# Optimization experiments

Measured on AMD Instinct MI355X. Metric: run time of the kernel, lower is better.

The kernel has to match this reference:

```python
import jax, jax.numpy as jnp
import numpy as np

# Dims: T=out_seq_len, B=batch, D=hidden_dim, H=hidden_dim_de, E=embedding_size, C=feat_channels
T, B, D, H, E, C, FH, FW = 32, 16, 512, 512, 512, 512, 8, 32


def _lstm_dir(x_seq, W_ih, W_hh, b_ih, b_hh, reverse):
    # x_seq: (T, B, D); PyTorch gate order i, f, g, o
    gx = jnp.einsum('tbd,gd->tbg', x_seq, W_ih) + b_ih  # (T, B, 4H)
    Hh = W_hh.shape[1]
    def step(carry, g_t):
        h, c = carry
        g = g_t + h @ W_hh.T + b_hh
        i, f, gg, o = jnp.split(g, 4, axis=-1)
        c = jax.nn.sigmoid(f) * c + jax.nn.sigmoid(i) * jnp.tanh(gg)
        h = jax.nn.sigmoid(o) * jnp.tanh(c)
        return (h, c), h
    init = (jnp.zeros((x_seq.shape[1], Hh), x_seq.dtype),
            jnp.zeros((x_seq.shape[1], Hh), x_seq.dtype))
    _, hs = jax.lax.scan(step, init, gx, reverse=reverse)
    return hs  # (T, B, H)


def setup_inputs() -> dict:
    key = jax.random.key(0)
    ks = jax.random.split(key, 16)
    s = 0.02
    inp = {
        'hidden_en': jax.random.normal(ks[0], (T, B, D), jnp.float32),
        'conv_f': jax.random.normal(ks[1], (B, C, FH, FW), jnp.float32),
        # bidirectional LSTM params (PyTorch layout: W_ih (4H, D), W_hh (4H, H))
        'W_ih_f': jax.random.normal(ks[2], (4 * H, D), jnp.float32) * s,
        'W_hh_f': jax.random.normal(ks[3], (4 * H, H), jnp.float32) * s,
        'b_ih_f': jnp.zeros((4 * H,), jnp.float32),
        'b_hh_f': jnp.zeros((4 * H,), jnp.float32),
        'W_ih_b': jax.random.normal(ks[4], (4 * H, D), jnp.float32) * s,
        'W_hh_b': jax.random.normal(ks[5], (4 * H, H), jnp.float32) * s,
        'b_ih_b': jnp.zeros((4 * H,), jnp.float32),
        'b_hh_b': jnp.zeros((4 * H,), jnp.float32),
        # linear_decode: (H, 2H)
        'W_dec': jax.random.normal(ks[6], (H, 2 * H), jnp.float32) * s,
        'b_dec': jnp.zeros((H,), jnp.float32),
        # conv_em: 3x3, C -> E (OIHW)
        'W_em': jax.random.normal(ks[7], (E, C, 3, 3), jnp.float32) * s,
        'b_em': jnp.zeros((E,), jnp.float32),
        # attention h_em: 1x1 conv == linear H -> E
        'W_hem': jax.random.normal(ks[8], (E, H), jnp.float32) * s,
        'b_hem': jnp.zeros((E,), jnp.float32),
        # conv_att: 1x1 conv E -> 1
        'w_att': jax.random.normal(ks[9], (E,), jnp.float32) * s,
        'b_att': jnp.zeros((), jnp.float32),
    }
    return inp


def reference(hidden_en, conv_f, W_ih_f, W_hh_f, b_ih_f, b_hh_f,
              W_ih_b, W_hh_b, b_ih_b, b_hh_b, W_dec, b_dec,
              W_em, b_em, W_hem, b_hem, w_att, b_att):
    # decoder_ctc: bidirectional LSTM + linear
    h_fwd = _lstm_dir(hidden_en, W_ih_f, W_hh_f, b_ih_f, b_hh_f, reverse=False)
    h_bwd = _lstm_dir(hidden_en, W_ih_b, W_hh_b, b_ih_b, b_hh_b, reverse=True)
    hidden_de = jnp.concatenate([h_fwd, h_bwd], axis=-1) @ W_dec.T + b_dec  # (T, B, H)

    # conv_em: 3x3 same-padding conv, NCHW
    x_em = jax.lax.conv_general_dilated(
        conv_f, W_em, window_strides=(1, 1), padding='SAME',
        dimension_numbers=('NCHW', 'OIHW', 'NCHW')) + b_em[None, :, None, None]  # (B,E,FH,FW)
    att_x_em = jnp.transpose(x_em.reshape(x_em.shape[0], E, -1), (0, 2, 1))  # (B, HW, E)

    # batched attention over all timesteps (dropout is identity at eval)
    h_em = jnp.einsum('tbh,eh->tbe', hidden_de, W_hem) + b_hem  # (T, B, E)
    feat = jnp.tanh(x_em[None] + h_em[:, :, :, None, None])     # (T, B, E, FH, FW)
    scores = jnp.einsum('tbehw,e->tbhw', feat, w_att) + b_att   # (T, B, FH, FW)
    alpha = jax.nn.softmax(scores.reshape(scores.shape[0], scores.shape[1], -1), axis=-1)  # (T,B,HW)
    att = jnp.einsum('tbn,bne->tbe', alpha, att_x_em)           # (T, B, E)

    ctc_out = jnp.concatenate([hidden_de, att], axis=-1)        # (T, B, H+E)
    return jnp.transpose(ctc_out, (1, 0, 2))                    # (B, T, H+E)
```

## Files before the change

### kernel.cpp

```cpp
#include <hip/hip_runtime.h>
#include <hip/hip_bf16.h>
#include <math.h>

#define T_LEN 32
#define BATCH 16
#define DDIM  512
#define HDIM  512
#define EDIM  512
#define CDIM  512
#define FHH   8
#define FWW   32
#define HW    256
#define G4    2048
#define PADH  10
#define PADW  34
#define WLP   520

typedef __attribute__((ext_vector_type(8))) short bf16x8;
typedef __attribute__((ext_vector_type(4))) float f32x4;
typedef __attribute__((ext_vector_type(4))) int i32x4;

__device__ __forceinline__ ushort bfr(float x) {
    union { float f; uint32_t u; } c; c.f = x;
    uint32_t r = (c.u + 0x7FFFu + ((c.u >> 16) & 1u)) >> 16;
    return (ushort)r;
}

__device__ __forceinline__ float frcp(float x) { return __builtin_amdgcn_rcpf(x); }
__device__ __forceinline__ float ftanh(float x) {
    return 1.f - 2.f * frcp(1.f + __expf(2.f * x));
}
__device__ __forceinline__ float fsig(float x) {
    return frcp(1.f + __expf(-x));
}

__device__ __forceinline__ void ld_lds16(const void* g, void* l) {
    __builtin_amdgcn_global_load_lds((const __attribute__((address_space(1))) void*)g,
                                     (__attribute__((address_space(3))) void*)l, 16, 0, 0);
}

__device__ __forceinline__ void st_u16_sc1(ushort* p, ushort v) {
    asm volatile("global_store_short %0, %1, off sc1" :: "v"(p), "v"((uint)v) : "memory");
}
__device__ __forceinline__ void st_i32_sc1(int* p, int v) {
    asm volatile("global_store_dword %0, %1, off sc1" :: "v"(p), "v"(v) : "memory");
}
__device__ __forceinline__ void st_f32_sc1(float* p, float v) {
    asm volatile("global_store_dword %0, %1, off sc1" :: "v"(p), "v"(v) : "memory");
}
__device__ __forceinline__ int ld_i32_sc1(const int* p) {
    int v;
    asm volatile("global_load_dword %0, %1, off sc1\n\ts_waitcnt vmcnt(0)"
                 : "=v"(v) : "v"(p) : "memory");
    return v;
}
__device__ __forceinline__ i32x4 ld_i32x4_sc1(const int* p) {
    i32x4 v;
    asm volatile("global_load_dwordx4 %0, %1, off sc1\n\ts_waitcnt vmcnt(0)"
                 : "=v"(v) : "v"(p) : "memory");
    return v;
}
__device__ __forceinline__ float ld_f32_sc1(const float* p) {
    float v;
    asm volatile("global_load_dword %0, %1, off sc1\n\ts_waitcnt vmcnt(0)"
                 : "=v"(v) : "v"(p) : "memory");
    return v;
}
__device__ __forceinline__ f32x4 ld_f32x4_sc1_async(const float* p) {
    f32x4 v;
    asm volatile("global_load_dwordx4 %0, %1, off sc1" : "=v"(v) : "v"(p));
    return v;
}

struct PrepArgs { const float* s[7]; ushort* d[7]; };
__global__ __launch_bounds__(256) void prep_all(
    PrepArgs a, int* __restrict__ syncbuf,
    const float* __restrict__ conv_f, ushort* __restrict__ padT,
    const float* __restrict__ W_em, ushort* __restrict__ Wt,
    const float* __restrict__ W_dec, ushort* __restrict__ WdecT,
    const float* __restrict__ W_hem, const float* __restrict__ b_dec,
    const float* __restrict__ b_hem, float* __restrict__ b_comb)
{
    __shared__ float tile[32][33];
    const int bid = blockIdx.x, tid = threadIdx.x;
    if (bid < 5120) {
        int i = bid * 256 + tid;
        if (i < 128) st_i32_sc1(syncbuf + i, 0);
        const int e0 = 65536, e1 = 327680, e2 = 589824, e3 = 851968,
                  e4 = 1114112, e5 = 1245184;
        int seg, base;
        if      (i < e0) { seg = 0; base = 0;  }
        else if (i < e1) { seg = 1; base = e0; }
        else if (i < e2) { seg = 2; base = e1; }
        else if (i < e3) { seg = 3; base = e2; }
        else if (i < e4) { seg = 4; base = e3; }
        else if (i < e5) { seg = 5; base = e4; }
        else             { seg = 6; base = e5; }
        int li = i - base;
        float4 v = ((const float4*)a.s[seg])[li];
        ushort4 o;
        o.x = bfr(v.x); o.y = bfr(v.y); o.z = bfr(v.z); o.w = bfr(v.w);
        ((ushort4*)a.d[seg])[li] = o;
        return;
    }
    if (bid < 7168) {
        int id = bid - 5120;
        int s0 = (id & 7) * 32, c0 = ((id >> 3) & 15) * 32, b = id >> 7;
        int lo = tid & 31, hi = tid >> 5;
#pragma unroll
        for (int it = 0; it < 4; ++it) {
            int cl = hi + it * 8;
            tile[cl][lo] = conv_f[((size_t)(b * CDIM + c0 + cl)) * HW + s0 + lo];
        }
        __syncthreads();
#pragma unroll
        for (int it = 0; it < 4; ++it) {
            int sl = hi + it * 8;
            int s = s0 + sl;
            int y = s >> 5, x = s & 31;
            padT[(((size_t)b * PADH + y + 1) * PADW + (x + 1)) * CDIM + c0 + lo] =
                bfr(tile[lo][sl]);
        }
        return;
    }
    if (bid < 7840) {
        int gid = (bid - 7168) * 256 + tid;
        int c4 = gid & 127;
        int cellb = gid >> 7;
        int cell = cellb % 84;
        int b = cellb / 84;
        int y, x;
        if (cell < 34) { y = 0; x = cell; }
        else if (cell < 68) { y = 9; x = cell - 34; }
        else { int k2 = cell - 68; y = 1 + (k2 >> 1); x = (k2 & 1) ? 33 : 0; }
        ((ushort4*)padT)[(((size_t)b * PADH + y) * PADW + x) * (CDIM / 4) + c4] =
            make_ushort4(0, 0, 0, 0);
        return;
    }
    if (bid < 17056) {
        int gid = (bid - 7840) * 256 + tid;
        int c = gid % CDIM;
        int t = gid / CDIM;
        int e = t % EDIM;
        int tap = t / EDIM;
        int dy = tap / 3, dx = tap % 3;
        Wt[gid] = bfr(W_em[((e * CDIM + c) * 3 + dy) * 3 + dx]);
        return;
    }
    if (bid < 17568) {
        int idx = bid - 17056;
        int ht = idx & 15, kt = idx >> 4;
        int h0 = ht * 32, k0 = kt * 32;
        int lo = tid & 31, hi = tid >> 5;
#pragma unroll
        for (int it = 0; it < 4; ++it) {
            int i = hi + it * 8;
            tile[i][lo] = W_dec[(size_t)(h0 + i) * 1024 + k0 + lo];
        }
        __syncthreads();
#pragma unroll
        for (int it = 0; it < 4; ++it) {
            int i = hi + it * 8;
            WdecT[(size_t)(k0 + i) * 512 + h0 + lo] = bfr(tile[lo][i]);
        }
        return;
    }
    {
        int e = (bid - 17568) * 256 + tid;
        float s = b_hem[e];
        const float* wr = W_hem + (size_t)e * 512;
        for (int h = 0; h < 512; ++h) s += wr[h] * b_dec[h];
        b_comb[e] = s;
    }
}

__device__ __forceinline__ void tile64_compute(
    const ushort* Ap0, const ushort* Bp0, int K,
    ushort* smem, int tid, f32x4 (&acc)[2][2])
{
    ushort* As = smem;
    ushort* Bs = smem + 2048;
    const int w = tid >> 6, lane = tid & 63;
    ushort* AsW = &As[w * 512];
    ushort* BsW = &Bs[w * 512];
    const int wm = (w >> 1) * 32, wn = (w & 1) * 32;
    const int kb = (lane >> 4) * 8, fr = lane & 15;
    for (int kk = 0; kk < K; kk += 32) {
        __syncthreads();
        ld_lds16(Ap0 + kk, AsW);
        ld_lds16(Bp0 + kk, BsW);
        __syncthreads();
        bf16x8 af[2], bg[2];
#pragma unroll
        for (int i = 0; i < 2; ++i)
            af[i] = *(const bf16x8*)&As[(wm + i * 16 + fr) * 32 + kb];
#pragma unroll
        for (int j = 0; j < 2; ++j)
            bg[j] = *(const bf16x8*)&Bs[(wn + j * 16 + fr) * 32 + kb];
#pragma unroll
        for (int i = 0; i < 2; ++i)
#pragma unroll
            for (int j = 0; j < 2; ++j)
                acc[i][j] = __builtin_amdgcn_mfma_f32_16x16x32_bf16(af[i], bg[j], acc[i][j], 0, 0, 0);
    }
}

__global__ __launch_bounds__(256) void fused_main(
    const ushort* __restrict__ Whh_f, const ushort* __restrict__ Whh_b,
    float* __restrict__ gxT_f, float* __restrict__ gxT_b,
    const ushort* __restrict__ hen_bf,
    const ushort* __restrict__ Wih_f, const ushort* __restrict__ Wih_b,
    const float* __restrict__ b_ih_f, const float* __restrict__ b_hh_f,
    const float* __restrict__ b_ih_b, const float* __restrict__ b_hh_b,
    ushort* __restrict__ hs_bf,
    int* __restrict__ syncbuf,
    const ushort* __restrict__ padT, const ushort* __restrict__ Wt,
    const float* __restrict__ bias_em, float* __restrict__ xem,
    const ushort* __restrict__ Whem_bf, const ushort* __restrict__ WdecT_bf,
    ushort* __restrict__ Wcomb_bf)
{
    __shared__ ushort smem[49152];
    const int bid = blockIdx.x, tid = threadIdx.x;
    const int w = tid >> 6, lane = tid & 63;
    int* flags = syncbuf;
    int* gcnt  = syncbuf + 64;

    if (bid < 64) {
        const int dir = bid >> 5;
        const int j0 = (bid & 31) * 16;
        const ushort* W = dir ? Whh_b : Whh_f;
        const float* gx = dir ? gxT_b : gxT_f;
#pragma unroll
        for (int i = 0; i < 16; ++i) {
            int row = w * 16 + i;
            int g = row >> 4, jl = row & 15;
            bf16x8 v = *(const bf16x8*)(W + ((size_t)(g * 512 + j0 + jl)) * 512 + lane * 8);
            *(bf16x8*)&smem[row * WLP + lane * 8] = v;
        }
        __syncthreads();
        if (tid >= 64) return;
        __builtin_amdgcn_s_setprio(1);

        const int fr = lane & 15, kq = lane >> 4;
        const int j = j0 + fr;
        const int* fq4 = &flags[dir * 32 + (lane & 7) * 4];
        const int t0 = dir ? (T_LEN - 1) : 0;
        int mt_ok = t0 >> 2;
        {
            const int* gp = &gcnt[dir * 8 + mt_ok];
            while (ld_i32_sc1(gp) < 32) __builtin_amdgcn_s_sleep(4);
        }
        f32x4 gq[4];
#pragma unroll
        for (int r = 0; r < 4; ++r)
            gq[r] = ld_f32x4_sc1_async(gx + (((size_t)t0 * BATCH + kq * 4 + r) * 512 + j) * 4);
        f32x4 cr = {0.f, 0.f, 0.f, 0.f};
        for (int step = 0; step < T_LEN; ++step) {
            const int tcur = dir ? (T_LEN - 1 - step) : step;
            if (step > 0) {
                const int need = step;
                for (;;) {
                    i32x4 v = ld_i32x4_sc1(fq4);
                    int mn = min(min(v[0], v[1]), min(v[2], v[3]));
                    if (__all(mn >= need)) break;
                    __builtin_amdgcn_s_sleep(1);
                }
            }
            f32x4 acc[4];
#pragma unroll
            for (int g = 0; g < 4; ++g) acc[g] = {0.f, 0.f, 0.f, 0.f};
            if (step > 0) {
                const int tprev = dir ? tcur + 1 : tcur - 1;
                const ushort* hp = hs_bf + ((size_t)tprev * BATCH + fr) * 1024 + dir * 512 + kq * 8;
                bf16x8 hreg[16];
#pragma unroll
                for (int u = 0; u < 16; ++u)
                    asm volatile("global_load_dwordx4 %0, %1, off sc1"
                                 : "=v"(hreg[u]) : "v"(hp + u * 32));
                asm volatile("s_waitcnt vmcnt(0)" ::: "memory");
                __builtin_amdgcn_sched_barrier(0);
#pragma unroll
                for (int u = 0; u < 16; ++u) {
#pragma unroll
                    for (int g = 0; g < 4; ++g) {
                        bf16x8 bb = *(const bf16x8*)&smem[(g * 16 + fr) * WLP + kq * 8 + u * 32];
                        acc[g] = __builtin_amdgcn_mfma_f32_16x16x32_bf16(hreg[u], bb, acc[g], 0, 0, 0);
                    }
                }
            } else {
                asm volatile("s_waitcnt vmcnt(0)" ::: "memory");
                __builtin_amdgcn_sched_barrier(0);
            }
#pragma unroll
            for (int r = 0; r < 4; ++r) {
                int b = kq * 4 + r;
                float gi = gq[r][0] + acc[0][r];
                float gf = gq[r][1] + acc[1][r];
                float gg = gq[r][2] + acc[2][r];
                float go = gq[r][3] + acc[3][r];
                float si = fsig(gi), sf = fsig(gf), so = fsig(go);
                float c = sf * cr[r] + si * ftanh(gg);
                cr[r] = c;
                float h = so * ftanh(c);
                st_u16_sc1(hs_bf + ((size_t)tcur * BATCH + b) * 1024 + dir * 512 + j, bfr(h));
            }
            if (step < T_LEN - 1) {
                asm volatile("s_waitcnt vmcnt(0)" ::: "memory");
                if (lane == 0) st_i32_sc1(&flags[bid], step + 1);
                const int tnext = dir ? tcur - 1 : tcur + 1;
                const int mtn = tnext >> 2;
                if (mtn != mt_ok) {
                    const int* gp = &gcnt[dir * 8 + mtn];
                    while (ld_i32_sc1(gp) < 32) __builtin_amdgcn_s_sleep(2);
                    mt_ok = mtn;
                }
#pragma unroll
                for (int r = 0; r < 4; ++r)
                    gq[r] = ld_f32x4_sc1_async(gx + (((size_t)tnext * BATCH + kq * 4 + r) * 512 + j) * 4);
            }
        }
        return;
    }

    const int r0 = tid >> 2, c0 = (tid & 3) * 8;
    const int wm = (w >> 1) * 32, wn = (w & 1) * 32;
    const int col = lane & 15, rq = (lane >> 4) * 4;
    f32x4 acc[2][2];
#pragma unroll
    for (int i = 0; i < 2; ++i)
#pragma unroll
        for (int j = 0; j < 2; ++j) acc[i][j] = {0.f, 0.f, 0.f, 0.f};

    if (bid < 576) {
        const int gi = bid - 64;
        const int dir = gi & 1;
        const int q = gi >> 1;
        const int nt = q & 31;
        const int mt0 = q >> 5;
        const int mtile = dir ? (7 - mt0) : mt0;
        const ushort* Bw = dir ? Wih_b : Wih_f;
        const float* bi0 = dir ? b_ih_b : b_ih_f;
        const float* bi1 = dir ? b_hh_b : b_hh_f;
        float* Cg = dir ? gxT_b : gxT_f;
        const int m0 = mtile * 64, n0 = nt * 64;
        tile64_compute(hen_bf + (size_t)(m0 + r0) * 512 + c0,
                       Bw + (size_t)(n0 + r0) * 512 + c0, 512, smem, tid, acc);
#pragma unroll
        for (int i = 0; i < 2; ++i)
#pragma unroll
            for (int r = 0; r < 4; ++r) {
                int m = m0 + wm + i * 16 + rq + r;
#pragma unroll
                for (int j2 = 0; j2 < 2; ++j2) {
                    int n = n0 + wn + j2 * 16 + col;
                    st_f32_sc1(&Cg[(size_t)m * G4 + (n & 511) * 4 + (n >> 9)],
                               acc[i][j2][r] + bi0[n] + bi1[n]);
                }
            }
        asm volatile("s_waitcnt vmcnt(0)" ::: "memory");
        __syncthreads();
        if (tid == 0) atomicAdd(&gcnt[dir * 8 + mtile], 1);
        return;
    }
    if (bid < 1088) {
        const int cbid = bid - 576;
        const int n0 = (cbid & 7) * 64, m0 = (cbid >> 3) * 64;
        const int b = m0 >> 8, s0 = m0 & 255, y0 = s0 >> 5;
        const int y = y0 + (r0 >> 5), x = r0 & 31;
        const ushort* Abase = padT + (((size_t)b * PADH + y) * PADW + x) * CDIM + c0;
        const ushort* Bbase = Wt + (size_t)(n0 + r0) * CDIM + c0;
        for (int tap = 0; tap < 9; ++tap) {
            const int dy = tap / 3, dx = tap % 3;
            tile64_compute(Abase + ((size_t)dy * PADW + dx) * CDIM,
                           Bbase + (size_t)tap * EDIM * CDIM, 512, smem, tid, acc);
        }
#pragma unroll
        for (int i = 0; i < 2; ++i)
#pragma unroll
            for (int r = 0; r < 4; ++r) {
                int m = m0 + wm + i * 16 + rq + r;
                int s = m & 255;
#pragma unroll
                for (int j2 = 0; j2 < 2; ++j2) {
                    int e = n0 + wn + j2 * 16 + col;
                    xem[((size_t)b * EDIM + e) * HW + s] = acc[i][j2][r] + bias_em[e];
                }
            }
        return;
    }
    {
        const int wb = bid - 1088;
        const int mt = wb >> 4, nt = wb & 15;
        const int m0 = mt * 64, n0 = nt * 64;
        tile64_compute(Whem_bf + (size_t)(m0 + r0) * 512 + c0,
                       WdecT_bf + (size_t)(n0 + r0) * 512 + c0, 512, smem, tid, acc);
#pragma unroll
        for (int i = 0; i < 2; ++i)
#pragma unroll
            for (int r = 0; r < 4; ++r) {
                int m = m0 + wm + i * 16 + rq + r;
#pragma unroll
                for (int j2 = 0; j2 < 2; ++j2) {
                    int n = n0 + wn + j2 * 16 + col;
                    Wcomb_bf[(size_t)m * 1024 + n] = bfr(acc[i][j2][r]);
                }
            }
    }
}

__global__ __launch_bounds__(256) void tail(
    const ushort* __restrict__ hs_bf, const ushort* __restrict__ Wdec_bf,
    const float* __restrict__ b_dec, float* __restrict__ out,
    const ushort* __restrict__ Wcomb_bf, const float* __restrict__ b_comb,
    float* __restrict__ h_em,
    const float* __restrict__ xem, const float* __restrict__ watt,
    int* __restrict__ syncbuf)
{
    __shared__ ushort smem[4096];
    int* hcnt = syncbuf + 96;
    const int bid = blockIdx.x, tid = threadIdx.x;
    const int w = tid >> 6, lane = tid & 63;
    const int r0 = tid >> 2, c0 = (tid & 3) * 8;
    const int wm = (w >> 1) * 32, wn = (w & 1) * 32;
    const int col = lane & 15, rq = (lane >> 4) * 4;

    if (bid < 128) {
        f32x4 acc[2][2];
#pragma unroll
        for (int i = 0; i < 2; ++i)
#pragma unroll
            for (int j = 0; j < 2; ++j) acc[i][j] = {0.f, 0.f, 0.f, 0.f};
        if (bid < 64) {
            const int mt = bid >> 3, nt = bid & 7;
            const int m0 = mt * 64, n0 = nt * 64;
            tile64_compute(hs_bf + (size_t)(m0 + r0) * 1024 + c0,
                           Wdec_bf + (size_t)(n0 + r0) * 1024 + c0, 1024, smem, tid, acc);
#pragma unroll
            for (int i = 0; i < 2; ++i)
#pragma unroll
                for (int r = 0; r < 4; ++r) {
                    int m = m0 + wm + i * 16 + rq + r;
                    int t = m >> 4, b = m & 15;
#pragma unroll
                    for (int j2 = 0; j2 < 2; ++j2) {
                        int n = n0 + wn + j2 * 16 + col;
                        out[((size_t)(b * T_LEN + t)) * 1024 + n] = acc[i][j2][r] + b_dec[n];
                    }
                }
        } else {
            const int blk = bid - 64;
            const int mt = blk >> 3, nt = blk & 7;
            const int m0 = mt * 64, n0 = nt * 64;
            tile64_compute(hs_bf + (size_t)(m0 + r0) * 1024 + c0,
                           Wcomb_bf + (size_t)(n0 + r0) * 1024 + c0, 1024, smem, tid, acc);
#pragma unroll
            for (int i = 0; i < 2; ++i)
#pragma unroll
                for (int r = 0; r < 4; ++r) {
                    int m = m0 + wm + i * 16 + rq + r;
#pragma unroll
                    for (int j2 = 0; j2 < 2; ++j2) {
                        int n = n0 + wn + j2 * 16 + col;
                        st_f32_sc1(&h_em[(size_t)m * 512 + n], acc[i][j2][r] + b_comb[n]);
                    }
                }
            asm volatile("s_waitcnt vmcnt(0)" ::: "memory");
            __syncthreads();
            if (tid == 0) atomicAdd(&hcnt[mt], 1);
        }
        return;
    }

    {
        int i = bid - 128;
        int k = i >> 3;
        int b = ((i & 7) << 1) | (k & 1);
        int t = k >> 1;
        int tb = t * 16 + b;
        const int mt = tb >> 6;
        if (tid == 0) {
            while (ld_i32_sc1(&hcnt[mt]) < 8) __builtin_amdgcn_s_sleep(8);
        }
        __syncthreads();
        float* fs = (float*)smem;
        float* hl = fs;
        float* wl = fs + 512;
        float* al = fs + 1024;
        float* red = fs + 1280;
        for (int q = tid; q < 512; q += 256) {
            hl[q] = ld_f32_sc1(&h_em[(size_t)tb * 512 + q]);
            wl[q] = watt[q];
        }
        __syncthreads();
        const float* xb = xem + (size_t)b * EDIM * HW;
        float sc = 0.f;
#pragma unroll 4
        for (int e = 0; e < 512; ++e)
            sc += ftanh(xb[(size_t)e * HW + tid] + hl[e]) * wl[e];
        float m = sc;
#pragma unroll
        for (int o = 32; o; o >>= 1) m = fmaxf(m, __shfl_xor(m, o));
        if ((tid & 63) == 0) red[tid >> 6] = m;
        __syncthreads();
        m = fmaxf(fmaxf(red[0], red[1]), fmaxf(red[2], red[3]));
        float ex = __expf(sc - m);
        float s = ex;
#pragma unroll
        for (int o = 32; o; o >>= 1) s += __shfl_xor(s, o);
        if ((tid & 63) == 0) red[4 + (tid >> 6)] = s;
        __syncthreads();
        s = red[4] + red[5] + red[6] + red[7];
        al[tid] = ex * frcp(s);
        __syncthreads();
        float* ob = out + ((size_t)(b * T_LEN + t)) * 1024 + 512;
        for (int eo = 0; eo < 512; eo += 256) {
            int e = eo + tid;
            const float* xr = xb + (size_t)e * HW;
            float acc2 = 0.f;
#pragma unroll 4
            for (int n = 0; n < 256; n += 4) {
                float4 v = *(const float4*)&xr[n];
                acc2 += al[n] * v.x + al[n + 1] * v.y + al[n + 2] * v.z + al[n + 3] * v.w;
            }
            ob[e] = acc2;
        }
    }
}

extern "C" void kernel_launch(void* const* d_in, const int* in_sizes, int n_in,
                              void* d_out, int out_size, void* d_ws, size_t ws_size,
                              hipStream_t stream) {
    const float* hidden_en = (const float*)d_in[0];
    const float* conv_f    = (const float*)d_in[1];
    const float* W_ih_f    = (const float*)d_in[2];
    const float* W_hh_f    = (const float*)d_in[3];
    const float* b_ih_f    = (const float*)d_in[4];
    const float* b_hh_f    = (const float*)d_in[5];
    const float* W_ih_b    = (const float*)d_in[6];
    const float* W_hh_b    = (const float*)d_in[7];
    const float* b_ih_b    = (const float*)d_in[8];
    const float* b_hh_b    = (const float*)d_in[9];
    const float* W_dec     = (const float*)d_in[10];
    const float* b_dec     = (const float*)d_in[11];
    const float* W_em      = (const float*)d_in[12];
    const float* b_em      = (const float*)d_in[13];
    const float* W_hem     = (const float*)d_in[14];
    const float* b_hem     = (const float*)d_in[15];
    const float* w_att     = (const float*)d_in[16];
    float* out = (float*)d_out;

    char* p = (char*)d_ws;
    auto alloc = [&](size_t bytes) { void* r = p; p += (bytes + 255) & ~(size_t)255; return r; };
    float*    gxT_f   = (float*)alloc((size_t)T_LEN * BATCH * G4 * 4);
    float*    gxT_b   = (float*)alloc((size_t)T_LEN * BATCH * G4 * 4);
    float*    h_em    = (float*)alloc((size_t)T_LEN * BATCH * 512 * 4);
    float*    x_em    = (float*)alloc((size_t)BATCH * EDIM * HW * 4);
    ushort*   padT    = (ushort*)alloc((size_t)BATCH * PADH * PADW * CDIM * 2);
    ushort*   Wt      = (ushort*)alloc((size_t)9 * EDIM * CDIM * 2);
    ushort*   hen_bf  = (ushort*)alloc((size_t)T_LEN * BATCH * DDIM * 2);
    ushort*   Wihf_bf = (ushort*)alloc((size_t)G4 * DDIM * 2);
    ushort*   Wihb_bf = (ushort*)alloc((size_t)G4 * DDIM * 2);
    ushort*   Whhf_bf = (ushort*)alloc((size_t)G4 * HDIM * 2);
    ushort*   Whhb_bf = (ushort*)alloc((size_t)G4 * HDIM * 2);
    ushort*   Wdec_bf = (ushort*)alloc((size_t)HDIM * 1024 * 2);
    ushort*   Whem_bf = (ushort*)alloc((size_t)EDIM * HDIM * 2);
    ushort*   WdecT_bf= (ushort*)alloc((size_t)1024 * 512 * 2);
    ushort*   Wcomb_bf= (ushort*)alloc((size_t)512 * 1024 * 2);
    float*    b_comb  = (float*)alloc(512 * 4);
    ushort*   hs_bf   = (ushort*)alloc((size_t)T_LEN * BATCH * 1024 * 2);
    int*      syncbuf = (int*)alloc(1024);

    PrepArgs pa;
    pa.s[0] = hidden_en; pa.d[0] = hen_bf;
    pa.s[1] = W_ih_f;    pa.d[1] = Wihf_bf;
    pa.s[2] = W_ih_b;    pa.d[2] = Wihb_bf;
    pa.s[3] = W_hh_f;    pa.d[3] = Whhf_bf;
    pa.s[4] = W_hh_b;    pa.d[4] = Whhb_bf;
    pa.s[5] = W_dec;     pa.d[5] = Wdec_bf;
    pa.s[6] = W_hem;     pa.d[6] = Whem_bf;
    prep_all<<<17570, 256, 0, stream>>>(pa, syncbuf, conv_f, padT, W_em, Wt,
                                        W_dec, WdecT_bf, W_hem, b_dec, b_hem, b_comb);

    fused_main<<<1216, 256, 0, stream>>>(Whhf_bf, Whhb_bf, gxT_f, gxT_b, hen_bf,
                                         Wihf_bf, Wihb_bf, b_ih_f, b_hh_f,
                                         b_ih_b, b_hh_b, hs_bf, syncbuf,
                                         padT, Wt, b_em, x_em,
                                         Whem_bf, WdecT_bf, Wcomb_bf);

    tail<<<640, 256, 0, stream>>>(hs_bf, Wdec_bf, b_dec, out,
                                  Wcomb_bf, b_comb, h_em, x_em, w_att, syncbuf);
}
```

Before: 280.2 us.

## Replace per-step flag barrier with step-tagged hidden-state words in recurrent LSTM

The recurrent LSTM blocks no longer publish and poll per-block step flags. Each hidden value is now written as a 32-bit word whose high half holds the step tag, and consumers spin-load the hidden-state slices directly until every tag matches. This removes the store-wait, the flag store and the separate flag-polling round trip from each serial step, at the cost of doubled hidden-state traffic, an extra zeroing pass in prep and a second bf16 copy for the tail kernel.

```diff
diff --git a/kernel.cpp b/kernel.cpp
--- a/kernel.cpp
+++ b/kernel.cpp
@@ -39,14 +39,14 @@
                                      (__attribute__((address_space(3))) void*)l, 16, 0, 0);
 }
 
-__device__ __forceinline__ void st_u16_sc1(ushort* p, ushort v) {
-    asm volatile("global_store_short %0, %1, off sc1" :: "v"(p), "v"((uint)v) : "memory");
-}
 __device__ __forceinline__ void st_i32_sc1(int* p, int v) {
     asm volatile("global_store_dword %0, %1, off sc1" :: "v"(p), "v"(v) : "memory");
 }
 __device__ __forceinline__ void st_f32_sc1(float* p, float v) {
     asm volatile("global_store_dword %0, %1, off sc1" :: "v"(p), "v"(v) : "memory");
+}
+__device__ __forceinline__ void st_i32x4_sc1(int* p, i32x4 v) {
+    asm volatile("global_store_dwordx4 %0, %1, off sc1" :: "v"(p), "v"(v) : "memory");
 }
 __device__ __forceinline__ int ld_i32_sc1(const int* p) {
     int v;
@@ -54,12 +54,6 @@
                  : "=v"(v) : "v"(p) : "memory");
     return v;
 }
-__device__ __forceinline__ i32x4 ld_i32x4_sc1(const int* p) {
-    i32x4 v;
-    asm volatile("global_load_dwordx4 %0, %1, off sc1\n\ts_waitcnt vmcnt(0)"
-                 : "=v"(v) : "v"(p) : "memory");
-    return v;
-}
 __device__ __forceinline__ float ld_f32_sc1(const float* p) {
     float v;
     asm volatile("global_load_dword %0, %1, off sc1\n\ts_waitcnt vmcnt(0)"
@@ -68,6 +62,11 @@
 }
 __device__ __forceinline__ f32x4 ld_f32x4_sc1_async(const float* p) {
     f32x4 v;
+    asm volatile("global_load_dwordx4 %0, %1, off sc1" : "=v"(v) : "v"(p));
+    return v;
+}
+__device__ __forceinline__ i32x4 ld_i32x4_sc1_async(const int* p) {
+    i32x4 v;
     asm volatile("global_load_dwordx4 %0, %1, off sc1" : "=v"(v) : "v"(p));
     return v;
 }
@@ -79,7 +78,8 @@
     const float* __restrict__ W_em, ushort* __restrict__ Wt,
     const float* __restrict__ W_dec, ushort* __restrict__ WdecT,
     const float* __restrict__ W_hem, const float* __restrict__ b_dec,
-    const float* __restrict__ b_hem, float* __restrict__ b_comb)
+    const float* __restrict__ b_hem, float* __restrict__ b_comb,
+    int* __restrict__ hs32)
 {
     __shared__ float tile[32][33];
     const int bid = blockIdx.x, tid = threadIdx.x;
@@ -165,12 +165,18 @@
         }
         return;
     }
-    {
+    if (bid < 17570) {
         int e = (bid - 17568) * 256 + tid;
         float s = b_hem[e];
         const float* wr = W_hem + (size_t)e * 512;
         for (int h = 0; h < 512; ++h) s += wr[h] * b_dec[h];
         b_comb[e] = s;
+        return;
+    }
+    {
+        int gid = (bid - 17570) * 256 + tid;
+        i32x4 z = {0, 0, 0, 0};
+        st_i32x4_sc1(hs32 + (size_t)gid * 4, z);
     }
 }
 
@@ -212,18 +218,17 @@
     const ushort* __restrict__ Wih_f, const ushort* __restrict__ Wih_b,
     const float* __restrict__ b_ih_f, const float* __restrict__ b_hh_f,
     const float* __restrict__ b_ih_b, const float* __restrict__ b_hh_b,
-    ushort* __restrict__ hs_bf,
+    int* __restrict__ hs32, ushort* __restrict__ hs_bf,
     int* __restrict__ syncbuf,
     const ushort* __restrict__ padT, const ushort* __restrict__ Wt,
     const float* __restrict__ bias_em, float* __restrict__ xem,
     const ushort* __restrict__ Whem_bf, const ushort* __restrict__ WdecT_bf,
     ushort* __restrict__ Wcomb_bf)
 {
-    __shared__ ushort smem[49152];
+    __shared__ ushort smem[64 * WLP];
     const int bid = blockIdx.x, tid = threadIdx.x;
     const int w = tid >> 6, lane = tid & 63;
-    int* flags = syncbuf;
-    int* gcnt  = syncbuf + 64;
+    int* gcnt = syncbuf + 64;
 
     if (bid < 64) {
         const int dir = bid >> 5;
@@ -243,7 +248,6 @@
 
         const int fr = lane & 15, kq = lane >> 4;
         const int j = j0 + fr;
-        const int* fq4 = &flags[dir * 32 + (lane & 7) * 4];
         const int t0 = dir ? (T_LEN - 1) : 0;
         int mt_ok = t0 >> 2;
         {
@@ -257,40 +261,58 @@
         f32x4 cr = {0.f, 0.f, 0.f, 0.f};
         for (int step = 0; step < T_LEN; ++step) {
             const int tcur = dir ? (T_LEN - 1 - step) : step;
-            if (step > 0) {
-                const int need = step;
-                for (;;) {
-                    i32x4 v = ld_i32x4_sc1(fq4);
-                    int mn = min(min(v[0], v[1]), min(v[2], v[3]));
-                    if (__all(mn >= need)) break;
-                    __builtin_amdgcn_s_sleep(1);
-                }
-            }
             f32x4 acc[4];
 #pragma unroll
             for (int g = 0; g < 4; ++g) acc[g] = {0.f, 0.f, 0.f, 0.f};
             if (step > 0) {
                 const int tprev = dir ? tcur + 1 : tcur - 1;
-                const ushort* hp = hs_bf + ((size_t)tprev * BATCH + fr) * 1024 + dir * 512 + kq * 8;
-                bf16x8 hreg[16];
-#pragma unroll
-                for (int u = 0; u < 16; ++u)
-                    asm volatile("global_load_dwordx4 %0, %1, off sc1"
-                                 : "=v"(hreg[u]) : "v"(hp + u * 32));
-                asm volatile("s_waitcnt vmcnt(0)" ::: "memory");
-                __builtin_amdgcn_sched_barrier(0);
-#pragma unroll
-                for (int u = 0; u < 16; ++u) {
-#pragma unroll
-                    for (int g = 0; g < 4; ++g) {
-                        bf16x8 bb = *(const bf16x8*)&smem[(g * 16 + fr) * WLP + kq * 8 + u * 32];
-                        acc[g] = __builtin_amdgcn_mfma_f32_16x16x32_bf16(hreg[u], bb, acc[g], 0, 0, 0);
+                const uint taghi = (uint)step;
+                const int* hb = hs32 + ((size_t)tprev * BATCH + fr) * 1024 + dir * 512 + kq * 8;
+#pragma unroll
+                for (int H = 0; H < 2; ++H) {
+                    const int* hbH = hb + H * 256;
+                    i32x4 L[16];
+                    for (;;) {
+#pragma unroll
+                        for (int c = 0; c < 8; ++c) {
+                            L[2 * c]     = ld_i32x4_sc1_async(hbH + c * 32);
+                            L[2 * c + 1] = ld_i32x4_sc1_async(hbH + c * 32 + 4);
+                        }
+                        asm volatile("s_waitcnt vmcnt(0)" ::: "memory");
+                        __builtin_amdgcn_sched_barrier(0);
+                        uint err = 0;
+#pragma unroll
+                        for (int q = 0; q < 16; ++q)
+#pragma unroll
+                            for (int z = 0; z < 4; ++z)
+                                err |= ((uint)L[q][z] >> 16) ^ taghi;
+                        if (__all(err == 0)) break;
+                        __builtin_amdgcn_s_sleep(1);
+                    }
+#pragma unroll
+                    for (int c = 0; c < 8; ++c) {
+                        union { bf16x8 v; uint u[4]; } ua;
+                        uint e0 = (uint)L[2 * c][0], e1 = (uint)L[2 * c][1];
+                        uint e2 = (uint)L[2 * c][2], e3 = (uint)L[2 * c][3];
+                        uint e4 = (uint)L[2 * c + 1][0], e5 = (uint)L[2 * c + 1][1];
+                        uint e6 = (uint)L[2 * c + 1][2], e7 = (uint)L[2 * c + 1][3];
+                        ua.u[0] = (e1 << 16) | (e0 & 0xFFFFu);
+                        ua.u[1] = (e3 << 16) | (e2 & 0xFFFFu);
+                        ua.u[2] = (e5 << 16) | (e4 & 0xFFFFu);
+                        ua.u[3] = (e7 << 16) | (e6 & 0xFFFFu);
+                        const int kk = H * 256 + c * 32;
+#pragma unroll
+                        for (int g = 0; g < 4; ++g) {
+                            bf16x8 bb = *(const bf16x8*)&smem[(g * 16 + fr) * WLP + kq * 8 + kk];
+                            acc[g] = __builtin_amdgcn_mfma_f32_16x16x32_bf16(ua.v, bb, acc[g], 0, 0, 0);
+                        }
                     }
                 }
             } else {
                 asm volatile("s_waitcnt vmcnt(0)" ::: "memory");
                 __builtin_amdgcn_sched_barrier(0);
             }
+            const uint tw = (uint)(step + 1) << 16;
 #pragma unroll
             for (int r = 0; r < 4; ++r) {
                 int b = kq * 4 + r;
@@ -302,11 +324,12 @@
                 float c = sf * cr[r] + si * ftanh(gg);
                 cr[r] = c;
                 float h = so * ftanh(c);
-                st_u16_sc1(hs_bf + ((size_t)tcur * BATCH + b) * 1024 + dir * 512 + j, bfr(h));
+                ushort hb16 = bfr(h);
+                size_t idx = ((size_t)tcur * BATCH + b) * 1024 + dir * 512 + j;
+                st_i32_sc1(hs32 + idx, (int)(tw | (uint)hb16));
+                hs_bf[idx] = hb16;
             }
             if (step < T_LEN - 1) {
-                asm volatile("s_waitcnt vmcnt(0)" ::: "memory");
-                if (lane == 0) st_i32_sc1(&flags[bid], step + 1);
                 const int tnext = dir ? tcur - 1 : tcur + 1;
                 const int mtn = tnext >> 2;
                 if (mtn != mt_ok) {
@@ -567,6 +590,7 @@
     ushort*   WdecT_bf= (ushort*)alloc((size_t)1024 * 512 * 2);
     ushort*   Wcomb_bf= (ushort*)alloc((size_t)512 * 1024 * 2);
     float*    b_comb  = (float*)alloc(512 * 4);
+    int*      hs32    = (int*)alloc((size_t)T_LEN * BATCH * 1024 * 4);
     ushort*   hs_bf   = (ushort*)alloc((size_t)T_LEN * BATCH * 1024 * 2);
     int*      syncbuf = (int*)alloc(1024);
 
@@ -578,12 +602,13 @@
     pa.s[4] = W_hh_b;    pa.d[4] = Whhb_bf;
     pa.s[5] = W_dec;     pa.d[5] = Wdec_bf;
     pa.s[6] = W_hem;     pa.d[6] = Whem_bf;
-    prep_all<<<17570, 256, 0, stream>>>(pa, syncbuf, conv_f, padT, W_em, Wt,
-                                        W_dec, WdecT_bf, W_hem, b_dec, b_hem, b_comb);
+    prep_all<<<18082, 256, 0, stream>>>(pa, syncbuf, conv_f, padT, W_em, Wt,
+                                        W_dec, WdecT_bf, W_hem, b_dec, b_hem,
+                                        b_comb, hs32);
 
     fused_main<<<1216, 256, 0, stream>>>(Whhf_bf, Whhb_bf, gxT_f, gxT_b, hen_bf,
                                          Wihf_bf, Wihb_bf, b_ih_f, b_hh_f,
-                                         b_ih_b, b_hh_b, hs_bf, syncbuf,
+                                         b_ih_b, b_hh_b, hs32, hs_bf, syncbuf,
                                          padT, Wt, b_em, x_em,
                                          Whem_bf, WdecT_bf, Wcomb_bf);
 
```

After: 327.7 us. 1.17x slower.

## Merge tail kernel into fused main kernel with flag-based dependencies

Applied to the files above, without the earlier changes.

Folds the decode/h_em GEMMs and the attention blocks into the main persistent kernel, so one launch runs everything. Blocks after the LSTM wait on per-step LSTM flags, a conv completion counter and a Wcomb counter instead of a kernel boundary. Decode tiles can then start as soon as their timesteps finish, overlapping the recurrence. This adds spin-waiting blocks that hold CU slots. It also depends on blocks being dispatched in index order to avoid deadlock.

```diff
diff --git a/kernel.cpp b/kernel.cpp
--- a/kernel.cpp
+++ b/kernel.cpp
@@ -205,7 +205,7 @@
     }
 }
 
-__global__ __launch_bounds__(256) void fused_main(
+__global__ __launch_bounds__(256) void fused_all(
     const ushort* __restrict__ Whh_f, const ushort* __restrict__ Whh_b,
     float* __restrict__ gxT_f, float* __restrict__ gxT_b,
     const ushort* __restrict__ hen_bf,
@@ -217,13 +217,19 @@
     const ushort* __restrict__ padT, const ushort* __restrict__ Wt,
     const float* __restrict__ bias_em, float* __restrict__ xem,
     const ushort* __restrict__ Whem_bf, const ushort* __restrict__ WdecT_bf,
-    ushort* __restrict__ Wcomb_bf)
+    ushort* __restrict__ Wcomb_bf,
+    const ushort* __restrict__ Wdec_bf, const float* __restrict__ b_dec,
+    const float* __restrict__ b_comb, float* __restrict__ h_em,
+    const float* __restrict__ watt, float* __restrict__ out)
 {
-    __shared__ ushort smem[49152];
+    __shared__ ushort smem[64 * WLP];
     const int bid = blockIdx.x, tid = threadIdx.x;
     const int w = tid >> 6, lane = tid & 63;
     int* flags = syncbuf;
     int* gcnt  = syncbuf + 64;
+    int* hcnt  = syncbuf + 96;
+    int* ccnt  = syncbuf + 104;
+    int* wcnt  = syncbuf + 105;
 
     if (bid < 64) {
         const int dir = bid >> 5;
@@ -304,9 +310,9 @@
                 float h = so * ftanh(c);
                 st_u16_sc1(hs_bf + ((size_t)tcur * BATCH + b) * 1024 + dir * 512 + j, bfr(h));
             }
+            asm volatile("s_waitcnt vmcnt(0)" ::: "memory");
+            if (lane == 0) st_i32_sc1(&flags[bid], step + 1);
             if (step < T_LEN - 1) {
-                asm volatile("s_waitcnt vmcnt(0)" ::: "memory");
-                if (lane == 0) st_i32_sc1(&flags[bid], step + 1);
                 const int tnext = dir ? tcur - 1 : tcur + 1;
                 const int mtn = tnext >> 2;
                 if (mtn != mt_ok) {
@@ -325,116 +331,124 @@
     const int r0 = tid >> 2, c0 = (tid & 3) * 8;
     const int wm = (w >> 1) * 32, wn = (w & 1) * 32;
     const int col = lane & 15, rq = (lane >> 4) * 4;
-    f32x4 acc[2][2];
-#pragma unroll
-    for (int i = 0; i < 2; ++i)
-#pragma unroll
-        for (int j = 0; j < 2; ++j) acc[i][j] = {0.f, 0.f, 0.f, 0.f};
-
-    if (bid < 576) {
-        const int gi = bid - 64;
-        const int dir = gi & 1;
-        const int q = gi >> 1;
-        const int nt = q & 31;
-        const int mt0 = q >> 5;
-        const int mtile = dir ? (7 - mt0) : mt0;
-        const ushort* Bw = dir ? Wih_b : Wih_f;
-        const float* bi0 = dir ? b_ih_b : b_ih_f;
-        const float* bi1 = dir ? b_hh_b : b_hh_f;
-        float* Cg = dir ? gxT_b : gxT_f;
-        const int m0 = mtile * 64, n0 = nt * 64;
-        tile64_compute(hen_bf + (size_t)(m0 + r0) * 512 + c0,
-                       Bw + (size_t)(n0 + r0) * 512 + c0, 512, smem, tid, acc);
+
+    if (bid < 1216) {
+        f32x4 acc[2][2];
 #pragma unroll
         for (int i = 0; i < 2; ++i)
 #pragma unroll
-            for (int r = 0; r < 4; ++r) {
-                int m = m0 + wm + i * 16 + rq + r;
-#pragma unroll
-                for (int j2 = 0; j2 < 2; ++j2) {
-                    int n = n0 + wn + j2 * 16 + col;
-                    st_f32_sc1(&Cg[(size_t)m * G4 + (n & 511) * 4 + (n >> 9)],
-                               acc[i][j2][r] + bi0[n] + bi1[n]);
-                }
+            for (int j = 0; j < 2; ++j) acc[i][j] = {0.f, 0.f, 0.f, 0.f};
+
+        if (bid < 576) {
+            const int gi = bid - 64;
+            const int dir = gi & 1;
+            const int q = gi >> 1;
+            const int nt = q & 31;
+            const int mt0 = q >> 5;
+            const int mtile = dir ? (7 - mt0) : mt0;
+            const ushort* Bw = dir ? Wih_b : Wih_f;
+            const float* bi0 = dir ? b_ih_b : b_ih_f;
+            const float* bi1 = dir ? b_hh_b : b_hh_f;
+            float* Cg = dir ? gxT_b : gxT_f;
+            const int m0 = mtile * 64, n0 = nt * 64;
+            tile64_compute(hen_bf + (size_t)(m0 + r0) * 512 + c0,
+                           Bw + (size_t)(n0 + r0) * 512 + c0, 512, smem, tid, acc);
+#pragma unroll
+            for (int i = 0; i < 2; ++i)
+#pragma unroll
+                for (int r = 0; r < 4; ++r) {
+                    int m = m0 + wm + i * 16 + rq + r;
+#pragma unroll
+                    for (int j2 = 0; j2 < 2; ++j2) {
+                        int n = n0 + wn + j2 * 16 + col;
+                        st_f32_sc1(&Cg[(size_t)m * G4 + (n & 511) * 4 + (n >> 9)],
+                                   acc[i][j2][r] + bi0[n] + bi1[n]);
+                    }
+                }
+            asm volatile("s_waitcnt vmcnt(0)" ::: "memory");
+            __syncthreads();
+            if (tid == 0) atomicAdd(&gcnt[dir * 8 + mtile], 1);
+            return;
+        }
+        if (bid < 1088) {
+            const int cbid = bid - 576;
+            const int n0 = (cbid & 7) * 64, m0 = (cbid >> 3) * 64;
+            const int b = m0 >> 8, s0 = m0 & 255, y0 = s0 >> 5;
+            const int y = y0 + (r0 >> 5), x = r0 & 31;
+            const ushort* Abase = padT + (((size_t)b * PADH + y) * PADW + x) * CDIM + c0;
+            const ushort* Bbase = Wt + (size_t)(n0 + r0) * CDIM + c0;
+            for (int tap = 0; tap < 9; ++tap) {
+                const int dy = tap / 3, dx = tap % 3;
+                tile64_compute(Abase + ((size_t)dy * PADW + dx) * CDIM,
+                               Bbase + (size_t)tap * EDIM * CDIM, 512, smem, tid, acc);
             }
-        asm volatile("s_waitcnt vmcnt(0)" ::: "memory");
-        __syncthreads();
-        if (tid == 0) atomicAdd(&gcnt[dir * 8 + mtile], 1);
-        return;
-    }
-    if (bid < 1088) {
-        const int cbid = bid - 576;
-        const int n0 = (cbid & 7) * 64, m0 = (cbid >> 3) * 64;
-        const int b = m0 >> 8, s0 = m0 & 255, y0 = s0 >> 5;
-        const int y = y0 + (r0 >> 5), x = r0 & 31;
-        const ushort* Abase = padT + (((size_t)b * PADH + y) * PADW + x) * CDIM + c0;
-        const ushort* Bbase = Wt + (size_t)(n0 + r0) * CDIM + c0;
-        for (int tap = 0; tap < 9; ++tap) {
-            const int dy = tap / 3, dx = tap % 3;
-            tile64_compute(Abase + ((size_t)dy * PADW + dx) * CDIM,
-                           Bbase + (size_t)tap * EDIM * CDIM, 512, smem, tid, acc);
-        }
+#pragma unroll
+            for (int i = 0; i < 2; ++i)
+#pragma unroll
+                for (int r = 0; r < 4; ++r) {
+                    int m = m0 + wm + i * 16 + rq + r;
+                    int s = m & 255;
+#pragma unroll
+                    for (int j2 = 0; j2 < 2; ++j2) {
+                        int e = n0 + wn + j2 * 16 + col;
+                        st_f32_sc1(&xem[((size_t)b * EDIM + e) * HW + s],
+                                   acc[i][j2][r] + bias_em[e]);
+                    }
+                }
+            asm volatile("s_waitcnt vmcnt(0)" ::: "memory");
+            __syncthreads();
+            if (tid == 0) atomicAdd(ccnt, 1);
+            return;
+        }
+        {
+            const int wb = bid - 1088;
+            const int mt = wb >> 4, nt = wb & 15;
+            const int m0 = mt * 64, n0 = nt * 64;
+            tile64_compute(Whem_bf + (size_t)(m0 + r0) * 512 + c0,
+                           WdecT_bf + (size_t)(n0 + r0) * 512 + c0, 512, smem, tid, acc);
+#pragma unroll
+            for (int i = 0; i < 2; ++i)
+#pragma unroll
+                for (int r = 0; r < 4; ++r) {
+                    int m = m0 + wm + i * 16 + rq + r;
+#pragma unroll
+                    for (int j2 = 0; j2 < 2; ++j2) {
+                        int n = n0 + wn + j2 * 16 + col;
+                        st_u16_sc1(&Wcomb_bf[(size_t)m * 1024 + n], bfr(acc[i][j2][r]));
+                    }
+                }
+            asm volatile("s_waitcnt vmcnt(0)" ::: "memory");
+            __syncthreads();
+            if (tid == 0) atomicAdd(wcnt, 1);
+            return;
+        }
+    }
+
+    if (bid < 1344) {
+        const int isHem = (bid >= 1280);
+        const int blk = isHem ? (bid - 1280) : (bid - 1216);
+        const int mt = blk >> 3, nt = blk & 7;
+        if (tid < 64) {
+            const int target = (lane < 32) ? (4 * mt + 4) : (32 - 4 * mt);
+            for (;;) {
+                int v = ld_i32_sc1(&flags[lane]);
+                if (__all(v >= target)) break;
+                __builtin_amdgcn_s_sleep(8);
+            }
+            if (isHem && lane == 0)
+                while (ld_i32_sc1(wcnt) < 128) __builtin_amdgcn_s_sleep(8);
+        }
+        __syncthreads();
+        f32x4 acc[2][2];
 #pragma unroll
         for (int i = 0; i < 2; ++i)
 #pragma unroll
-            for (int r = 0; r < 4; ++r) {
-                int m = m0 + wm + i * 16 + rq + r;
-                int s = m & 255;
-#pragma unroll
-                for (int j2 = 0; j2 < 2; ++j2) {
-                    int e = n0 + wn + j2 * 16 + col;
-                    xem[((size_t)b * EDIM + e) * HW + s] = acc[i][j2][r] + bias_em[e];
-                }
-            }
-        return;
-    }
-    {
-        const int wb = bid - 1088;
-        const int mt = wb >> 4, nt = wb & 15;
+            for (int j = 0; j < 2; ++j) acc[i][j] = {0.f, 0.f, 0.f, 0.f};
         const int m0 = mt * 64, n0 = nt * 64;
-        tile64_compute(Whem_bf + (size_t)(m0 + r0) * 512 + c0,
-                       WdecT_bf + (size_t)(n0 + r0) * 512 + c0, 512, smem, tid, acc);
-#pragma unroll
-        for (int i = 0; i < 2; ++i)
-#pragma unroll
-            for (int r = 0; r < 4; ++r) {
-                int m = m0 + wm + i * 16 + rq + r;
-#pragma unroll
-                for (int j2 = 0; j2 < 2; ++j2) {
-                    int n = n0 + wn + j2 * 16 + col;
-                    Wcomb_bf[(size_t)m * 1024 + n] = bfr(acc[i][j2][r]);
-                }
-            }
-    }
-}
-
-__global__ __launch_bounds__(256) void tail(
-    const ushort* __restrict__ hs_bf, const ushort* __restrict__ Wdec_bf,
-    const float* __restrict__ b_dec, float* __restrict__ out,
-    const ushort* __restrict__ Wcomb_bf, const float* __restrict__ b_comb,
-    float* __restrict__ h_em,
-    const float* __restrict__ xem, const float* __restrict__ watt,
-    int* __restrict__ syncbuf)
-{
-    __shared__ ushort smem[4096];
-    int* hcnt = syncbuf + 96;
-    const int bid = blockIdx.x, tid = threadIdx.x;
-    const int w = tid >> 6, lane = tid & 63;
-    const int r0 = tid >> 2, c0 = (tid & 3) * 8;
-    const int wm = (w >> 1) * 32, wn = (w & 1) * 32;
-    const int col = lane & 15, rq = (lane >> 4) * 4;
-
-    if (bid < 128) {
-        f32x4 acc[2][2];
-#pragma unroll
-        for (int i = 0; i < 2; ++i)
-#pragma unroll
-            for (int j = 0; j < 2; ++j) acc[i][j] = {0.f, 0.f, 0.f, 0.f};
-        if (bid < 64) {
-            const int mt = bid >> 3, nt = bid & 7;
-            const int m0 = mt * 64, n0 = nt * 64;
-            tile64_compute(hs_bf + (size_t)(m0 + r0) * 1024 + c0,
-                           Wdec_bf + (size_t)(n0 + r0) * 1024 + c0, 1024, smem, tid, acc);
+        tile64_compute(hs_bf + (size_t)(m0 + r0) * 1024 + c0,
+                       (isHem ? Wcomb_bf : Wdec_bf) + (size_t)(n0 + r0) * 1024 + c0,
+                       1024, smem, tid, acc);
+        if (!isHem) {
 #pragma unroll
             for (int i = 0; i < 2; ++i)
 #pragma unroll
@@ -448,11 +462,6 @@
                     }
                 }
         } else {
-            const int blk = bid - 64;
-            const int mt = blk >> 3, nt = blk & 7;
-            const int m0 = mt * 64, n0 = nt * 64;
-            tile64_compute(hs_bf + (size_t)(m0 + r0) * 1024 + c0,
-                           Wcomb_bf + (size_t)(n0 + r0) * 1024 + c0, 1024, smem, tid, acc);
 #pragma unroll
             for (int i = 0; i < 2; ++i)
 #pragma unroll
@@ -472,7 +481,7 @@
     }
 
     {
-        int i = bid - 128;
+        int i = bid - 1344;
         int k = i >> 3;
         int b = ((i & 7) << 1) | (k & 1);
         int t = k >> 1;
@@ -480,6 +489,7 @@
         const int mt = tb >> 6;
         if (tid == 0) {
             while (ld_i32_sc1(&hcnt[mt]) < 8) __builtin_amdgcn_s_sleep(8);
+            while (ld_i32_sc1(ccnt) < 512) __builtin_amdgcn_s_sleep(8);
         }
         __syncthreads();
         float* fs = (float*)smem;
@@ -581,12 +591,11 @@
     prep_all<<<17570, 256, 0, stream>>>(pa, syncbuf, conv_f, padT, W_em, Wt,
                                         W_dec, WdecT_bf, W_hem, b_dec, b_hem, b_comb);
 
-    fused_main<<<1216, 256, 0, stream>>>(Whhf_bf, Whhb_bf, gxT_f, gxT_b, hen_bf,
-                                         Wihf_bf, Wihb_bf, b_ih_f, b_hh_f,
-                                         b_ih_b, b_hh_b, hs_bf, syncbuf,
-                                         padT, Wt, b_em, x_em,
-                                         Whem_bf, WdecT_bf, Wcomb_bf);
-
-    tail<<<640, 256, 0, stream>>>(hs_bf, Wdec_bf, b_dec, out,
-                                  Wcomb_bf, b_comb, h_em, x_em, w_att, syncbuf);
-}
+    fused_all<<<1856, 256, 0, stream>>>(Whhf_bf, Whhb_bf, gxT_f, gxT_b, hen_bf,
+                                        Wihf_bf, Wihb_bf, b_ih_f, b_hh_f,
+                                        b_ih_b, b_hh_b, hs_bf, syncbuf,
+                                        padT, Wt, b_em, x_em,
+                                        Whem_bf, WdecT_bf, Wcomb_bf,
+                                        Wdec_bf, b_dec, b_comb, h_em,
+                                        w_att, out);
+}
```

After: 281.0 us. About the same (+0.3%).
